# Optimization experiments

Hardware: AMD Instinct MI355X
Metric: run time of the kernel (lower is better)

The kernel has to match this reference:

```python
import jax, jax.numpy as jnp
import numpy as np

PATCH_SIZE = 7
STRIDE = 1
ALPHA = 0.05


def _extract_patches(img):
    # img: [b, c, h, w] -> [b, N, D] with D = c * p * p, N = h'*w' (VALID unfold)
    patches = jax.lax.conv_general_dilated_patches(
        img,
        filter_shape=(PATCH_SIZE, PATCH_SIZE),
        window_strides=(STRIDE, STRIDE),
        padding='VALID',
    )  # [b, c*p*p, h', w']
    b, D = patches.shape[0], patches.shape[1]
    return patches.reshape(b, D, -1).transpose(0, 2, 1)  # [b, N, D]


def _coherence_one(xp, yp):
    # xp: [N, D] input patches, yp: [M, D] target patches
    # dist[j, i] = mean_d (xp[i, d] - yp[j, d])^2, via GEMM expansion
    D = xp.shape[1]
    x2 = jnp.sum(xp * xp, axis=1)  # [N]
    y2 = jnp.sum(yp * yp, axis=1)  # [M]
    cross = yp @ xp.T              # [M, N]
    dist = (y2[:, None] + x2[None, :] - 2.0 * cross) / D
    dist = jnp.maximum(dist, 0.0)  # guard tiny negatives from GEMM expansion
    # normalize each row by (row-min + alpha), then column-min, then mean
    row_min = jnp.min(dist, axis=1, keepdims=True)  # [M, 1]
    dist = dist / (row_min + ALPHA)
    return jnp.mean(jnp.min(dist, axis=0))


def setup_inputs() -> dict:
    key = jax.random.key(0)
    k1, k2 = jax.random.split(key)
    x = jax.random.normal(k1, (4, 3, 96, 96), dtype=jnp.float32)
    y = jax.random.normal(k2, (4, 3, 96, 96), dtype=jnp.float32)
    return {"x": x, "y": y}


def reference(x, y):
    xp = _extract_patches(x)  # [b, N, D]
    yp = _extract_patches(y)  # [b, M, D]
    per_image = jax.vmap(_coherence_one)(xp, yp)  # [b]
    return jnp.mean(per_image)  # batch_reduction='mean'
```

## Files before the change

kernel.cpp:

```cpp
#include <hip/hip_runtime.h>
#include <hip/hip_bf16.h>
#include <stdint.h>

#define IMG_H 96
#define IMG_W 96
#define IMG_C 3
#define HO    90
#define NPAT  8100
#define NPAD  8192
#define DDIM  147
#define KPAD  160
#define NCHK  5
#define BATCH 4
#define TILE  128
#define NT    (NPAD / TILE)
#define ALPHA 0.05f

typedef __attribute__((ext_vector_type(8))) short short8;
typedef __attribute__((ext_vector_type(4))) float f32x4;

__device__ __forceinline__ void async16(const void* g, void* l) {
    __builtin_amdgcn_global_load_lds(
        (const __attribute__((address_space(1))) unsigned int*)g,
        (__attribute__((address_space(3))) unsigned int*)l,
        16, 0, 0);
}

__global__ __launch_bounds__(256) void extract_patches(
    const float* __restrict__ img,
    __hip_bfloat16* __restrict__ pat,
    float* __restrict__ nrm,
    float* __restrict__ outzero)
{
    int wid  = threadIdx.x >> 6;
    int lane = threadIdx.x & 63;
    int pidx = blockIdx.x * 4 + wid;
    int b    = blockIdx.y;
    if (pidx >= NPAD) return;
    if (outzero && blockIdx.x == 0 && blockIdx.y == 0 && threadIdx.x == 0)
        outzero[0] = 0.f;
    const float* im = img + (size_t)b * (IMG_C * IMG_H * IMG_W);
    __hip_bfloat16* pp = pat + ((size_t)b * NPAD + pidx) * KPAD;
    int r = pidx / HO, c = pidx - r * HO;
    bool valid = pidx < NPAT;
    float ss = 0.f;
    for (int d = lane; d < KPAD; d += 64) {
        float v = 0.f;
        if (valid && d < DDIM) {
            int ch  = d / 49;
            int rem = d - ch * 49;
            int pr  = rem / 7, pc = rem - pr * 7;
            v = im[ch * (IMG_H * IMG_W) + (r + pr) * IMG_W + (c + pc)];
        }
        pp[d] = __float2bfloat16(v);
        ss += v * v;
    }
    for (int s = 32; s; s >>= 1) ss += __shfl_down(ss, s);
    if (lane == 0) nrm[(size_t)b * NPAD + pidx] = ss;
}

__global__ __launch_bounds__(256) void prep_rms(
    const float* __restrict__ row_min, float* __restrict__ rms)
{
    int i = blockIdx.x * 256 + threadIdx.x;
    if (i < BATCH * NPAD) {
        int j = i & (NPAD - 1);
        float rm = row_min[i];
        rms[i] = (j < NPAT) ? (1.0f / (float)DDIM) / (rm + ALPHA)
                            : __builtin_inff();
    }
}

template <int PASS>
__global__ __launch_bounds__(512, 2) void panel_pass(
    const __hip_bfloat16* __restrict__ Xp,
    const __hip_bfloat16* __restrict__ Yp,
    const float* __restrict__ x2,
    const float* __restrict__ y2,
    const float* __restrict__ rms,
    float* __restrict__ row_min,
    float* __restrict__ out)
{
    __shared__ __align__(16) __hip_bfloat16 S[2][NCHK * TILE * 32];
    __shared__ float sm_a[2][TILE];
    __shared__ float sm_b[2][TILE];
    __shared__ float pnl[TILE];
    __shared__ float red[4][TILE];

    int blk = blockIdx.x;
    int bz  = blk & 3;
    int tP  = blk >> 2;
    int tid = threadIdx.x;
    int wid = tid >> 6, lane = tid & 63;
    int wp  = wid >> 2;
    int ws  = wid & 3;

    const __hip_bfloat16* Pbase =
        (PASS == 1 ? Yp : Xp) + ((size_t)bz * NPAD + tP * TILE) * KPAD;
    const __hip_bfloat16* Sbase =
        (PASS == 1 ? Xp : Yp) + (size_t)bz * NPAD * KPAD;
    const float* pnl_src = (PASS == 1 ? y2 : x2) + (size_t)bz * NPAD + tP * TILE;
    const float* sma_src = (PASS == 1 ? x2 : y2) + (size_t)bz * NPAD;
    const float* smb_src = rms + (size_t)bz * NPAD;

    auto stageS = [&](int buf, const __hip_bfloat16* gsrc) {
        int row  = wid * 16 + (lane >> 2);
        int slog = (lane & 3) ^ ((row >> 1) & 3);
        const __hip_bfloat16* src = gsrc + (size_t)row * KPAD + slog * 8;
        __hip_bfloat16* dbase = &S[buf][wid * 512];
        for (int c = 0; c < NCHK; ++c)
            async16(src + c * 32, dbase + c * 4096);
    };
    auto stage_small = [&](int buf, int t) {
        if (wid == 0 && lane < 32)
            async16(sma_src + (size_t)t * TILE + lane * 4, &sm_a[buf][0]);
        if (PASS == 2 && wid == 4 && lane < 32)
            async16(smb_src + (size_t)t * TILE + lane * 4, &sm_b[buf][0]);
    };

    stageS(1, Pbase);
    stageS(0, Sbase);
    stage_small(0, 0);
    if (wid == 2 && lane < 32) async16(pnl_src + lane * 4, &pnl[0]);
    __syncthreads();

    int fr    = lane & 15;
    int sread = ((lane >> 4) ^ ((lane >> 1) & 3)) * 8;
    int prow  = wp * 64 + fr;

    short8 p_reg[NCHK][4];
#pragma unroll
    for (int c = 0; c < NCHK; ++c)
#pragma unroll
        for (int m = 0; m < 4; ++m)
            p_reg[c][m] =
                *(const short8*)&S[1][c * 4096 + (prow + m * 16) * 32 + sread];

    float xv[4];
    if (PASS == 2)
#pragma unroll
        for (int nb = 0; nb < 4; ++nb) xv[nb] = pnl[wp * 64 + nb * 16 + fr];

    __syncthreads();

    float runmin[PASS == 1 ? 16 : 4];
#pragma unroll
    for (int i = 0; i < (PASS == 1 ? 16 : 4); ++i)
        runmin[i] = __builtin_inff();

    int srow = ws * 32 + fr;

#pragma unroll 1
    for (int t = 0; t < NT; ++t) {
        int cur = t & 1;
        if (t + 1 < NT) {
            stageS(cur ^ 1, Sbase + (size_t)(t + 1) * TILE * KPAD);
            stage_small(cur ^ 1, t + 1);
        }

        if (PASS == 1) {
            f32x4 acc[4][2] = {};
#pragma unroll
            for (int c = 0; c < NCHK; ++c) {
                short8 s0 = *(const short8*)&S[cur][c * 4096 + srow * 32 + sread];
                short8 s1 = *(const short8*)&S[cur][c * 4096 + (srow + 16) * 32 + sread];
#pragma unroll
                for (int m = 0; m < 4; ++m) {
                    acc[m][0] = __builtin_amdgcn_mfma_f32_16x16x32_bf16(
                        p_reg[c][m], s0, acc[m][0], 0, 0, 0);
                    acc[m][1] = __builtin_amdgcn_mfma_f32_16x16x32_bf16(
                        p_reg[c][m], s1, acc[m][1], 0, 0, 0);
                }
            }
            int gcb = t * TILE;
            float xvn[2];
#pragma unroll
            for (int n = 0; n < 2; ++n) {
                int ic = ws * 32 + n * 16 + fr;
                xvn[n] = (gcb + ic < NPAT) ? sm_a[cur][ic] : __builtin_inff();
            }
#pragma unroll
            for (int m = 0; m < 4; ++m)
#pragma unroll
                for (int reg = 0; reg < 4; ++reg)
#pragma unroll
                    for (int n = 0; n < 2; ++n)
                        runmin[m * 4 + reg] = fminf(runmin[m * 4 + reg],
                            fmaf(-2.0f, acc[m][n][reg], xvn[n]));
        } else {
            f32x4 acc[2][4] = {};
#pragma unroll
            for (int c = 0; c < NCHK; ++c) {
                short8 s0 = *(const short8*)&S[cur][c * 4096 + srow * 32 + sread];
                short8 s1 = *(const short8*)&S[cur][c * 4096 + (srow + 16) * 32 + sread];
#pragma unroll
                for (int nb = 0; nb < 4; ++nb) {
                    acc[0][nb] = __builtin_amdgcn_mfma_f32_16x16x32_bf16(
                        s0, p_reg[c][nb], acc[0][nb], 0, 0, 0);
                    acc[1][nb] = __builtin_amdgcn_mfma_f32_16x16x32_bf16(
                        s1, p_reg[c][nb], acc[1][nb], 0, 0, 0);
                }
            }
#pragma unroll
            for (int ma = 0; ma < 2; ++ma)
#pragma unroll
                for (int reg = 0; reg < 4; ++reg) {
                    int jl = ws * 32 + ma * 16 + (lane >> 4) * 4 + reg;
                    float yv = sm_a[cur][jl];
                    float rr = sm_b[cur][jl];
#pragma unroll
                    for (int nb = 0; nb < 4; ++nb)
                        runmin[nb] = fminf(runmin[nb],
                            fmaf(-2.0f, acc[ma][nb][reg], yv + xv[nb]) * rr);
                }
        }
        __syncthreads();
    }

    if (PASS == 1) {
#pragma unroll
        for (int m = 0; m < 4; ++m)
#pragma unroll
            for (int reg = 0; reg < 4; ++reg) {
                float v = runmin[m * 4 + reg];
                for (int s = 1; s < 16; s <<= 1)
                    v = fminf(v, __shfl_xor(v, s));
                if ((lane & 15) == 0)
                    red[ws][wp * 64 + m * 16 + (lane >> 4) * 4 + reg] = v;
            }
        __syncthreads();
        if (tid < TILE) {
            float mv = fminf(fminf(red[0][tid], red[1][tid]),
                             fminf(red[2][tid], red[3][tid]));
            float rm = fmaxf(pnl[tid] + mv, 0.f) * (1.0f / (float)DDIM);
            row_min[(size_t)bz * NPAD + tP * TILE + tid] = rm;
        }
    } else {
#pragma unroll
        for (int nb = 0; nb < 4; ++nb) {
            float v = runmin[nb];
            v = fminf(v, __shfl_xor(v, 16));
            v = fminf(v, __shfl_xor(v, 32));
            if (lane < 16) red[ws][wp * 64 + nb * 16 + lane] = v;
        }
        __syncthreads();
        if (tid < TILE) {
            int gc = tP * TILE + tid;
            float cv = fminf(fminf(red[0][tid], red[1][tid]),
                             fminf(red[2][tid], red[3][tid]));
            cv = fmaxf(cv, 0.f);
            red[0][tid] = (gc < NPAT) ? cv : 0.f;
        }
        __syncthreads();
        if (tid < 64) {
            float s = red[0][tid] + red[0][tid + 64];
            for (int o = 32; o; o >>= 1) s += __shfl_down(s, o);
            if (tid == 0)
                atomicAdd(out, s * (1.0f / (float)(BATCH * NPAT)));
        }
    }
}

extern "C" void kernel_launch(void* const* d_in, const int* in_sizes, int n_in,
                              void* d_out, int out_size, void* d_ws, size_t ws_size,
                              hipStream_t stream) {
    const float* x = (const float*)d_in[0];
    const float* y = (const float*)d_in[1];
    float* out = (float*)d_out;

    char* ws = (char*)d_ws;
    size_t patSz = (size_t)BATCH * NPAD * KPAD * sizeof(__hip_bfloat16);
    __hip_bfloat16* Xp = (__hip_bfloat16*)ws;
    __hip_bfloat16* Yp = (__hip_bfloat16*)(ws + patSz);
    float* x2 = (float*)(ws + 2 * patSz);
    float* y2 = x2 + BATCH * NPAD;
    float* row_min = y2 + BATCH * NPAD;
    float* rms = row_min + BATCH * NPAD;

    dim3 eg(NPAD / 4, BATCH);
    extract_patches<<<eg, 256, 0, stream>>>(x, Xp, x2, out);
    extract_patches<<<eg, 256, 0, stream>>>(y, Yp, y2, nullptr);

    panel_pass<1><<<NT * BATCH, 512, 0, stream>>>(Xp, Yp, x2, y2, rms,
                                                  row_min, out);
    prep_rms<<<(BATCH * NPAD) / 256, 256, 0, stream>>>(row_min, rms);
    panel_pass<2><<<NT * BATCH, 512, 0, stream>>>(Xp, Yp, x2, y2, rms,
                                                  row_min, out);
}
```

Before: 225.9 us.

## Embed norms in patch padding and triple-buffer panel tiles with split barriers

Squared norms and the row normalisation factor are packed as hi/lo bf16 pairs into the unused pad columns of each patch row, so the panel kernels get them from the same LDS tile instead of doing separate small async loads. The main loop moves from double to triple buffering, using explicit vmcnt waits and a single raw barrier per iteration instead of syncthreads. It also raises wave priority around the MFMA block. The cost is more LDS per block, which may lower occupancy, and a small precision loss from the two-bf16 encoding of the norms.

```diff
diff --git a/kernel.cpp b/kernel.cpp
--- a/kernel.cpp
+++ b/kernel.cpp
@@ -15,6 +15,8 @@
 #define TILE  128
 #define NT    (NPAD / TILE)
 #define ALPHA 0.05f
+#define EBY 148
+#define EBX 152
 
 typedef __attribute__((ext_vector_type(8))) short short8;
 typedef __attribute__((ext_vector_type(4))) float f32x4;
@@ -26,10 +28,21 @@
         16, 0, 0);
 }
 
+__device__ __forceinline__ unsigned enc_pair(float v) {
+    unsigned hb = __float_as_uint(v) >> 16;
+    float lo = v - __uint_as_float(hb << 16);
+    unsigned lb = __float_as_uint(lo) >> 16;
+    return hb | (lb << 16);
+}
+__device__ __forceinline__ float dec_pair(unsigned u) {
+    return __uint_as_float(u << 16) + __uint_as_float(u & 0xFFFF0000u);
+}
+
 __global__ __launch_bounds__(256) void extract_patches(
     const float* __restrict__ img,
     __hip_bfloat16* __restrict__ pat,
     float* __restrict__ nrm,
+    int eb,
     float* __restrict__ outzero)
 {
     int wid  = threadIdx.x >> 6;
@@ -52,22 +65,25 @@
             int pr  = rem / 7, pc = rem - pr * 7;
             v = im[ch * (IMG_H * IMG_W) + (r + pr) * IMG_W + (c + pc)];
         }
-        pp[d] = __float2bfloat16(v);
+        if (d < eb || d >= eb + 2) pp[d] = __float2bfloat16(v);
         ss += v * v;
     }
     for (int s = 32; s; s >>= 1) ss += __shfl_down(ss, s);
-    if (lane == 0) nrm[(size_t)b * NPAD + pidx] = ss;
+    if (lane == 0) {
+        nrm[(size_t)b * NPAD + pidx] = ss;
+        *(unsigned*)&pp[eb] = enc_pair(ss);
+    }
 }
 
 __global__ __launch_bounds__(256) void prep_rms(
-    const float* __restrict__ row_min, float* __restrict__ rms)
+    const float* __restrict__ row_min, __hip_bfloat16* __restrict__ Yp)
 {
     int i = blockIdx.x * 256 + threadIdx.x;
     if (i < BATCH * NPAD) {
         int j = i & (NPAD - 1);
-        float rm = row_min[i];
-        rms[i] = (j < NPAT) ? (1.0f / (float)DDIM) / (rm + ALPHA)
-                            : __builtin_inff();
+        float v = (j < NPAT) ? (1.0f / (float)DDIM) / (row_min[i] + ALPHA)
+                             : 1e30f;
+        *(unsigned*)&Yp[(size_t)i * KPAD + 150] = enc_pair(v);
     }
 }
 
@@ -75,16 +91,11 @@
 __global__ __launch_bounds__(512, 2) void panel_pass(
     const __hip_bfloat16* __restrict__ Xp,
     const __hip_bfloat16* __restrict__ Yp,
-    const float* __restrict__ x2,
     const float* __restrict__ y2,
-    const float* __restrict__ rms,
     float* __restrict__ row_min,
     float* __restrict__ out)
 {
-    __shared__ __align__(16) __hip_bfloat16 S[2][NCHK * TILE * 32];
-    __shared__ float sm_a[2][TILE];
-    __shared__ float sm_b[2][TILE];
-    __shared__ float pnl[TILE];
+    __shared__ __align__(16) __hip_bfloat16 S[3][NCHK * TILE * 32];
     __shared__ float red[4][TILE];
 
     int blk = blockIdx.x;
@@ -99,9 +110,6 @@
         (PASS == 1 ? Yp : Xp) + ((size_t)bz * NPAD + tP * TILE) * KPAD;
     const __hip_bfloat16* Sbase =
         (PASS == 1 ? Xp : Yp) + (size_t)bz * NPAD * KPAD;
-    const float* pnl_src = (PASS == 1 ? y2 : x2) + (size_t)bz * NPAD + tP * TILE;
-    const float* sma_src = (PASS == 1 ? x2 : y2) + (size_t)bz * NPAD;
-    const float* smb_src = rms + (size_t)bz * NPAD;
 
     auto stageS = [&](int buf, const __hip_bfloat16* gsrc) {
         int row  = wid * 16 + (lane >> 2);
@@ -111,22 +119,18 @@
         for (int c = 0; c < NCHK; ++c)
             async16(src + c * 32, dbase + c * 4096);
     };
-    auto stage_small = [&](int buf, int t) {
-        if (wid == 0 && lane < 32)
-            async16(sma_src + (size_t)t * TILE + lane * 4, &sm_a[buf][0]);
-        if (PASS == 2 && wid == 4 && lane < 32)
-            async16(smb_src + (size_t)t * TILE + lane * 4, &sm_b[buf][0]);
-    };
-
-    stageS(1, Pbase);
+
+    stageS(2, Pbase);
     stageS(0, Sbase);
-    stage_small(0, 0);
-    if (wid == 2 && lane < 32) async16(pnl_src + lane * 4, &pnl[0]);
-    __syncthreads();
+    stageS(1, Sbase + (size_t)TILE * KPAD);
+    asm volatile("s_waitcnt vmcnt(10)" ::: "memory");
+    __builtin_amdgcn_s_barrier();
+    __builtin_amdgcn_sched_barrier(0);
 
     int fr    = lane & 15;
     int sread = ((lane >> 4) ^ ((lane >> 1) & 3)) * 8;
     int prow  = wp * 64 + fr;
+    int srow  = ws * 32 + fr;
 
     short8 p_reg[NCHK][4];
 #pragma unroll
@@ -134,36 +138,44 @@
 #pragma unroll
         for (int m = 0; m < 4; ++m)
             p_reg[c][m] =
-                *(const short8*)&S[1][c * 4096 + (prow + m * 16) * 32 + sread];
+                *(const short8*)&S[2][c * 4096 + (prow + m * 16) * 32 + sread];
 
     float xv[4];
     if (PASS == 2)
 #pragma unroll
-        for (int nb = 0; nb < 4; ++nb) xv[nb] = pnl[wp * 64 + nb * 16 + fr];
-
-    __syncthreads();
+        for (int nb = 0; nb < 4; ++nb) {
+            int pr = wp * 64 + nb * 16 + fr;
+            unsigned u = *(const unsigned*)
+                &S[2][4 * 4096 + pr * 32 + (3 ^ ((pr >> 1) & 3)) * 8];
+            xv[nb] = dec_pair(u);
+        }
+
+    asm volatile("s_waitcnt lgkmcnt(0)" ::: "memory");
+    __builtin_amdgcn_sched_barrier(0);
 
     float runmin[PASS == 1 ? 16 : 4];
 #pragma unroll
     for (int i = 0; i < (PASS == 1 ? 16 : 4); ++i)
         runmin[i] = __builtin_inff();
 
-    int srow = ws * 32 + fr;
-
 #pragma unroll 1
     for (int t = 0; t < NT; ++t) {
-        int cur = t & 1;
-        if (t + 1 < NT) {
-            stageS(cur ^ 1, Sbase + (size_t)(t + 1) * TILE * KPAD);
-            stage_small(cur ^ 1, t + 1);
-        }
+        if (t == NT - 1) asm volatile("s_waitcnt vmcnt(0)" ::: "memory");
+        else             asm volatile("s_waitcnt vmcnt(5)" ::: "memory");
+        __builtin_amdgcn_s_barrier();
+        __builtin_amdgcn_sched_barrier(0);
+        if (t + 2 < NT)
+            stageS((t + 2) % 3, Sbase + (size_t)(t + 2) * TILE * KPAD);
+
+        const __hip_bfloat16* Sc = &S[t % 3][0];
 
         if (PASS == 1) {
             f32x4 acc[4][2] = {};
+            __builtin_amdgcn_s_setprio(1);
 #pragma unroll
             for (int c = 0; c < NCHK; ++c) {
-                short8 s0 = *(const short8*)&S[cur][c * 4096 + srow * 32 + sread];
-                short8 s1 = *(const short8*)&S[cur][c * 4096 + (srow + 16) * 32 + sread];
+                short8 s0 = *(const short8*)&Sc[c * 4096 + srow * 32 + sread];
+                short8 s1 = *(const short8*)&Sc[c * 4096 + (srow + 16) * 32 + sread];
 #pragma unroll
                 for (int m = 0; m < 4; ++m) {
                     acc[m][0] = __builtin_amdgcn_mfma_f32_16x16x32_bf16(
@@ -172,12 +184,15 @@
                         p_reg[c][m], s1, acc[m][1], 0, 0, 0);
                 }
             }
+            __builtin_amdgcn_s_setprio(0);
             int gcb = t * TILE;
             float xvn[2];
 #pragma unroll
             for (int n = 0; n < 2; ++n) {
                 int ic = ws * 32 + n * 16 + fr;
-                xvn[n] = (gcb + ic < NPAT) ? sm_a[cur][ic] : __builtin_inff();
+                unsigned u = *(const unsigned*)
+                    &Sc[4 * 4096 + ic * 32 + (3 ^ ((ic >> 1) & 3)) * 8];
+                xvn[n] = (gcb + ic < NPAT) ? dec_pair(u) : __builtin_inff();
             }
 #pragma unroll
             for (int m = 0; m < 4; ++m)
@@ -189,10 +204,11 @@
                             fmaf(-2.0f, acc[m][n][reg], xvn[n]));
         } else {
             f32x4 acc[2][4] = {};
+            __builtin_amdgcn_s_setprio(1);
 #pragma unroll
             for (int c = 0; c < NCHK; ++c) {
-                short8 s0 = *(const short8*)&S[cur][c * 4096 + srow * 32 + sread];
-                short8 s1 = *(const short8*)&S[cur][c * 4096 + (srow + 16) * 32 + sread];
+                short8 s0 = *(const short8*)&Sc[c * 4096 + srow * 32 + sread];
+                short8 s1 = *(const short8*)&Sc[c * 4096 + (srow + 16) * 32 + sread];
 #pragma unroll
                 for (int nb = 0; nb < 4; ++nb) {
                     acc[0][nb] = __builtin_amdgcn_mfma_f32_16x16x32_bf16(
@@ -201,20 +217,22 @@
                         s1, p_reg[c][nb], acc[1][nb], 0, 0, 0);
                 }
             }
+            __builtin_amdgcn_s_setprio(0);
 #pragma unroll
             for (int ma = 0; ma < 2; ++ma)
 #pragma unroll
                 for (int reg = 0; reg < 4; ++reg) {
                     int jl = ws * 32 + ma * 16 + (lane >> 4) * 4 + reg;
-                    float yv = sm_a[cur][jl];
-                    float rr = sm_b[cur][jl];
+                    const unsigned* pq = (const unsigned*)
+                        &Sc[4 * 4096 + jl * 32 + (2 ^ ((jl >> 1) & 3)) * 8 + 4];
+                    float yv = dec_pair(pq[0]);
+                    float rr = dec_pair(pq[1]);
 #pragma unroll
                     for (int nb = 0; nb < 4; ++nb)
                         runmin[nb] = fminf(runmin[nb],
                             fmaf(-2.0f, acc[ma][nb][reg], yv + xv[nb]) * rr);
                 }
         }
-        __syncthreads();
     }
 
     if (PASS == 1) {
@@ -232,8 +250,9 @@
         if (tid < TILE) {
             float mv = fminf(fminf(red[0][tid], red[1][tid]),
                              fminf(red[2][tid], red[3][tid]));
-            float rm = fmaxf(pnl[tid] + mv, 0.f) * (1.0f / (float)DDIM);
-            row_min[(size_t)bz * NPAD + tP * TILE + tid] = rm;
+            float y2g = y2[(size_t)bz * NPAD + tP * TILE + tid];
+            row_min[(size_t)bz * NPAD + tP * TILE + tid] =
+                fmaxf(y2g + mv, 0.f) * (1.0f / (float)DDIM);
         }
     } else {
 #pragma unroll
@@ -275,15 +294,12 @@
     float* x2 = (float*)(ws + 2 * patSz);
     float* y2 = x2 + BATCH * NPAD;
     float* row_min = y2 + BATCH * NPAD;
-    float* rms = row_min + BATCH * NPAD;
 
     dim3 eg(NPAD / 4, BATCH);
-    extract_patches<<<eg, 256, 0, stream>>>(x, Xp, x2, out);
-    extract_patches<<<eg, 256, 0, stream>>>(y, Yp, y2, nullptr);
-
-    panel_pass<1><<<NT * BATCH, 512, 0, stream>>>(Xp, Yp, x2, y2, rms,
-                                                  row_min, out);
-    prep_rms<<<(BATCH * NPAD) / 256, 256, 0, stream>>>(row_min, rms);
-    panel_pass<2><<<NT * BATCH, 512, 0, stream>>>(Xp, Yp, x2, y2, rms,
-                                                  row_min, out);
-}
+    extract_patches<<<eg, 256, 0, stream>>>(x, Xp, x2, EBX, out);
+    extract_patches<<<eg, 256, 0, stream>>>(y, Yp, y2, EBY, nullptr);
+
+    panel_pass<1><<<NT * BATCH, 512, 0, stream>>>(Xp, Yp, y2, row_min, out);
+    prep_rms<<<(BATCH * NPAD) / 256, 256, 0, stream>>>(row_min, Yp);
+    panel_pass<2><<<NT * BATCH, 512, 0, stream>>>(Xp, Yp, y2, row_min, out);
+}
```

Result: slower. 257.3 us (+13.9%).

## Double waves per panel block to 16 and pack y2 with row scale

Applied to the files above, without the earlier changes.

The panel kernels move from 512 to 1024 threads. Each wave now covers 16 streamed rows instead of 32, so per-wave MFMA work and accumulator registers are halved, and the cross-wave min reduction goes over 8 partials. prep_rms now writes y2 and the row-normalisation factor interleaved as float2, so pass 2 stages and reads one array instead of two. The aim is more latency hiding with fewer registers per wave; the cost is that each wave holds the same panel registers for half the work, plus more LDS reads per MFMA and heavier barriers.

```diff
diff --git a/kernel.cpp b/kernel.cpp
--- a/kernel.cpp
+++ b/kernel.cpp
@@ -60,73 +60,81 @@
 }
 
 __global__ __launch_bounds__(256) void prep_rms(
-    const float* __restrict__ row_min, float* __restrict__ rms)
+    const float* __restrict__ row_min, const float* __restrict__ y2,
+    float2* __restrict__ yr)
 {
     int i = blockIdx.x * 256 + threadIdx.x;
     if (i < BATCH * NPAD) {
         int j = i & (NPAD - 1);
         float rm = row_min[i];
-        rms[i] = (j < NPAT) ? (1.0f / (float)DDIM) / (rm + ALPHA)
-                            : __builtin_inff();
+        float rr = (j < NPAT) ? (1.0f / (float)DDIM) / (rm + ALPHA)
+                              : __builtin_inff();
+        yr[i] = make_float2(y2[i], rr);
     }
 }
 
 template <int PASS>
-__global__ __launch_bounds__(512, 2) void panel_pass(
+__global__ __launch_bounds__(1024) void panel_pass(
     const __hip_bfloat16* __restrict__ Xp,
     const __hip_bfloat16* __restrict__ Yp,
     const float* __restrict__ x2,
     const float* __restrict__ y2,
-    const float* __restrict__ rms,
+    const float2* __restrict__ yr,
     float* __restrict__ row_min,
     float* __restrict__ out)
 {
     __shared__ __align__(16) __hip_bfloat16 S[2][NCHK * TILE * 32];
-    __shared__ float sm_a[2][TILE];
-    __shared__ float sm_b[2][TILE];
-    __shared__ float pnl[TILE];
-    __shared__ float red[4][TILE];
+    __shared__ __align__(16) float  sm_a[2][TILE];
+    __shared__ __align__(16) float2 sm_yr[2][TILE];
+    __shared__ __align__(16) float  pnl[TILE];
+    __shared__ float red[8][TILE];
 
     int blk = blockIdx.x;
     int bz  = blk & 3;
     int tP  = blk >> 2;
     int tid = threadIdx.x;
     int wid = tid >> 6, lane = tid & 63;
-    int wp  = wid >> 2;
-    int ws  = wid & 3;
+    int wp  = wid >> 3;
+    int ws  = wid & 7;
 
     const __hip_bfloat16* Pbase =
         (PASS == 1 ? Yp : Xp) + ((size_t)bz * NPAD + tP * TILE) * KPAD;
     const __hip_bfloat16* Sbase =
         (PASS == 1 ? Xp : Yp) + (size_t)bz * NPAD * KPAD;
     const float* pnl_src = (PASS == 1 ? y2 : x2) + (size_t)bz * NPAD + tP * TILE;
-    const float* sma_src = (PASS == 1 ? x2 : y2) + (size_t)bz * NPAD;
-    const float* smb_src = rms + (size_t)bz * NPAD;
+    const float*  sma_src = x2 + (size_t)bz * NPAD;
+    const float2* syr_src = yr + (size_t)bz * NPAD;
 
     auto stageS = [&](int buf, const __hip_bfloat16* gsrc) {
-        int row  = wid * 16 + (lane >> 2);
-        int slog = (lane & 3) ^ ((row >> 1) & 3);
-        const __hip_bfloat16* src = gsrc + (size_t)row * KPAD + slog * 8;
-        __hip_bfloat16* dbase = &S[buf][wid * 512];
-        for (int c = 0; c < NCHK; ++c)
-            async16(src + c * 32, dbase + c * 4096);
+        if (wid < 8) {
+            int row  = wid * 16 + (lane >> 2);
+            int slog = (lane & 3) ^ ((row >> 1) & 3);
+            const __hip_bfloat16* src = gsrc + (size_t)row * KPAD + slog * 8;
+            __hip_bfloat16* dbase = &S[buf][wid * 512];
+            for (int c = 0; c < NCHK; ++c)
+                async16(src + c * 32, dbase + c * 4096);
+        }
     };
     auto stage_small = [&](int buf, int t) {
-        if (wid == 0 && lane < 32)
-            async16(sma_src + (size_t)t * TILE + lane * 4, &sm_a[buf][0]);
-        if (PASS == 2 && wid == 4 && lane < 32)
-            async16(smb_src + (size_t)t * TILE + lane * 4, &sm_b[buf][0]);
+        if (PASS == 1) {
+            if (wid == 8 && lane < 32)
+                async16(sma_src + (size_t)t * TILE + lane * 4, &sm_a[buf][0]);
+        } else {
+            if (wid == 8)
+                async16(syr_src + (size_t)t * TILE + lane * 2, &sm_yr[buf][0]);
+        }
     };
 
     stageS(1, Pbase);
     stageS(0, Sbase);
     stage_small(0, 0);
-    if (wid == 2 && lane < 32) async16(pnl_src + lane * 4, &pnl[0]);
+    if (wid == 9 && lane < 32) async16(pnl_src + lane * 4, &pnl[0]);
     __syncthreads();
 
     int fr    = lane & 15;
     int sread = ((lane >> 4) ^ ((lane >> 1) & 3)) * 8;
     int prow  = wp * 64 + fr;
+    int srow  = ws * 16 + fr;
 
     short8 p_reg[NCHK][4];
 #pragma unroll
@@ -147,8 +155,6 @@
 #pragma unroll
     for (int i = 0; i < (PASS == 1 ? 16 : 4); ++i)
         runmin[i] = __builtin_inff();
-
-    int srow = ws * 32 + fr;
 
 #pragma unroll 1
     for (int t = 0; t < NT; ++t) {
@@ -158,61 +164,45 @@
             stage_small(cur ^ 1, t + 1);
         }
 
+        const __hip_bfloat16* Sc = &S[cur][0];
+
+        f32x4 acc[4] = {};
+#pragma unroll
+        for (int c = 0; c < NCHK; ++c) {
+            short8 s0 = *(const short8*)&Sc[c * 4096 + srow * 32 + sread];
+            if (PASS == 1) {
+#pragma unroll
+                for (int m = 0; m < 4; ++m)
+                    acc[m] = __builtin_amdgcn_mfma_f32_16x16x32_bf16(
+                        p_reg[c][m], s0, acc[m], 0, 0, 0);
+            } else {
+#pragma unroll
+                for (int nb = 0; nb < 4; ++nb)
+                    acc[nb] = __builtin_amdgcn_mfma_f32_16x16x32_bf16(
+                        s0, p_reg[c][nb], acc[nb], 0, 0, 0);
+            }
+        }
+
         if (PASS == 1) {
-            f32x4 acc[4][2] = {};
-#pragma unroll
-            for (int c = 0; c < NCHK; ++c) {
-                short8 s0 = *(const short8*)&S[cur][c * 4096 + srow * 32 + sread];
-                short8 s1 = *(const short8*)&S[cur][c * 4096 + (srow + 16) * 32 + sread];
-#pragma unroll
-                for (int m = 0; m < 4; ++m) {
-                    acc[m][0] = __builtin_amdgcn_mfma_f32_16x16x32_bf16(
-                        p_reg[c][m], s0, acc[m][0], 0, 0, 0);
-                    acc[m][1] = __builtin_amdgcn_mfma_f32_16x16x32_bf16(
-                        p_reg[c][m], s1, acc[m][1], 0, 0, 0);
-                }
+            int ic = ws * 16 + fr;
+            float xx = sm_a[cur][ic];
+            float xvn = (t * TILE + ic < NPAT) ? xx : __builtin_inff();
+#pragma unroll
+            for (int m = 0; m < 4; ++m)
+#pragma unroll
+                for (int reg = 0; reg < 4; ++reg)
+                    runmin[m * 4 + reg] = fminf(runmin[m * 4 + reg],
+                        fmaf(-2.0f, acc[m][reg], xvn));
+        } else {
+#pragma unroll
+            for (int reg = 0; reg < 4; ++reg) {
+                int jl = ws * 16 + (lane >> 4) * 4 + reg;
+                float2 p = sm_yr[cur][jl];
+#pragma unroll
+                for (int nb = 0; nb < 4; ++nb)
+                    runmin[nb] = fminf(runmin[nb],
+                        fmaf(-2.0f, acc[nb][reg], p.x + xv[nb]) * p.y);
             }
-            int gcb = t * TILE;
-            float xvn[2];
-#pragma unroll
-            for (int n = 0; n < 2; ++n) {
-                int ic = ws * 32 + n * 16 + fr;
-                xvn[n] = (gcb + ic < NPAT) ? sm_a[cur][ic] : __builtin_inff();
-            }
-#pragma unroll
-            for (int m = 0; m < 4; ++m)
-#pragma unroll
-                for (int reg = 0; reg < 4; ++reg)
-#pragma unroll
-                    for (int n = 0; n < 2; ++n)
-                        runmin[m * 4 + reg] = fminf(runmin[m * 4 + reg],
-                            fmaf(-2.0f, acc[m][n][reg], xvn[n]));
-        } else {
-            f32x4 acc[2][4] = {};
-#pragma unroll
-            for (int c = 0; c < NCHK; ++c) {
-                short8 s0 = *(const short8*)&S[cur][c * 4096 + srow * 32 + sread];
-                short8 s1 = *(const short8*)&S[cur][c * 4096 + (srow + 16) * 32 + sread];
-#pragma unroll
-                for (int nb = 0; nb < 4; ++nb) {
-                    acc[0][nb] = __builtin_amdgcn_mfma_f32_16x16x32_bf16(
-                        s0, p_reg[c][nb], acc[0][nb], 0, 0, 0);
-                    acc[1][nb] = __builtin_amdgcn_mfma_f32_16x16x32_bf16(
-                        s1, p_reg[c][nb], acc[1][nb], 0, 0, 0);
-                }
-            }
-#pragma unroll
-            for (int ma = 0; ma < 2; ++ma)
-#pragma unroll
-                for (int reg = 0; reg < 4; ++reg) {
-                    int jl = ws * 32 + ma * 16 + (lane >> 4) * 4 + reg;
-                    float yv = sm_a[cur][jl];
-                    float rr = sm_b[cur][jl];
-#pragma unroll
-                    for (int nb = 0; nb < 4; ++nb)
-                        runmin[nb] = fminf(runmin[nb],
-                            fmaf(-2.0f, acc[ma][nb][reg], yv + xv[nb]) * rr);
-                }
         }
         __syncthreads();
     }
@@ -230,10 +220,11 @@
             }
         __syncthreads();
         if (tid < TILE) {
-            float mv = fminf(fminf(red[0][tid], red[1][tid]),
-                             fminf(red[2][tid], red[3][tid]));
-            float rm = fmaxf(pnl[tid] + mv, 0.f) * (1.0f / (float)DDIM);
-            row_min[(size_t)bz * NPAD + tP * TILE + tid] = rm;
+            float mv = red[0][tid];
+#pragma unroll
+            for (int w = 1; w < 8; ++w) mv = fminf(mv, red[w][tid]);
+            row_min[(size_t)bz * NPAD + tP * TILE + tid] =
+                fmaxf(pnl[tid] + mv, 0.f) * (1.0f / (float)DDIM);
         }
     } else {
 #pragma unroll
@@ -246,8 +237,9 @@
         __syncthreads();
         if (tid < TILE) {
             int gc = tP * TILE + tid;
-            float cv = fminf(fminf(red[0][tid], red[1][tid]),
-                             fminf(red[2][tid], red[3][tid]));
+            float cv = red[0][tid];
+#pragma unroll
+            for (int w = 1; w < 8; ++w) cv = fminf(cv, red[w][tid]);
             cv = fmaxf(cv, 0.f);
             red[0][tid] = (gc < NPAT) ? cv : 0.f;
         }
@@ -275,15 +267,15 @@
     float* x2 = (float*)(ws + 2 * patSz);
     float* y2 = x2 + BATCH * NPAD;
     float* row_min = y2 + BATCH * NPAD;
-    float* rms = row_min + BATCH * NPAD;
+    float2* yr = (float2*)(row_min + BATCH * NPAD);
 
     dim3 eg(NPAD / 4, BATCH);
     extract_patches<<<eg, 256, 0, stream>>>(x, Xp, x2, out);
     extract_patches<<<eg, 256, 0, stream>>>(y, Yp, y2, nullptr);
 
-    panel_pass<1><<<NT * BATCH, 512, 0, stream>>>(Xp, Yp, x2, y2, rms,
-                                                  row_min, out);
-    prep_rms<<<(BATCH * NPAD) / 256, 256, 0, stream>>>(row_min, rms);
-    panel_pass<2><<<NT * BATCH, 512, 0, stream>>>(Xp, Yp, x2, y2, rms,
-                                                  row_min, out);
-}
+    panel_pass<1><<<NT * BATCH, 1024, 0, stream>>>(Xp, Yp, x2, y2, yr,
+                                                   row_min, out);
+    prep_rms<<<(BATCH * NPAD) / 256, 256, 0, stream>>>(row_min, y2, yr);
+    panel_pass<2><<<NT * BATCH, 1024, 0, stream>>>(Xp, Yp, x2, y2, yr,
+                                                   row_min, out);
+}
```

New measurement: 258.2 us. 1.14x slower.
